# Kernel optimization log

Hardware: AMD Instinct MI355X
Metric: run time of the kernel (lower is better)

The kernel has to match this reference:

```python
import jax, jax.numpy as jnp
import numpy as np

HID = 768  # hidden_size; feature dim is 2*HID


def setup_inputs() -> dict:
    key = jax.random.key(0)
    k1, k2 = jax.random.split(key)
    B, N, K, total_Q, D = 4, 10, 5, 512, 2 * HID
    support = jax.random.normal(k1, (B, N, K, D), dtype=jnp.float32)
    query = jax.random.normal(k2, (B, total_Q, D), dtype=jnp.float32)
    return {"support": support, "query": query, "N": N, "K": K, "total_Q": total_Q}


def reference(support, query, N, K, total_Q):
    B = support.shape[0]
    D = support.shape[-1]
    # (B, N*K, D)
    S = support.reshape(B, N * K, D)
    # negative squared euclidean distance: broadcast (B,1,NK,D) vs (B,Q,1,D) -> (B,Q,NK)
    dist_sq = -jnp.sum((S[:, None, :, :] - query[:, :, None, :]) ** 2, axis=3)
    dist_sq = dist_sq.reshape(B, total_Q, N, K)
    # query-guided weights: mean over queries, tanh, softmax over K -> (B,N,K,1)
    qgw = jax.nn.softmax(jnp.tanh(jnp.mean(dist_sq, axis=1)), axis=-1)[..., None]
    # weighted aggregation over shots -> (B,N,D)
    agg = jnp.sum(support * qgw, axis=2)
    return agg, qgw
```

## Files before the change

### kernel.cpp

```cpp
#include <hip/hip_runtime.h>
#include <math.h>

constexpr int B = 4;
constexpr int N = 10;
constexpr int K = 5;
constexpr int Q = 512;
constexpr int D = 1536;

constexpr int QBAR_OFF = 0;
constexpr int CSUM_OFF = B * D;

__global__ __launch_bounds__(256) void qstats_kernel(
    const float* __restrict__ query, float* __restrict__ ws) {
    const int tid = threadIdx.x;
    const int d   = blockIdx.y * 256 + tid;
    const int b   = blockIdx.z;
    const int q0  = blockIdx.x * 64;

    const float* qp = query + (size_t)b * Q * D + (size_t)q0 * D + d;
    float acc = 0.f, ssq = 0.f;
#pragma unroll 8
    for (int q = 0; q < 64; ++q) {
        float v = qp[(size_t)q * D];
        acc += v;
        ssq = fmaf(v, v, ssq);
    }
    atomicAdd(&ws[QBAR_OFF + b * D + d], acc);

    for (int off = 32; off > 0; off >>= 1) ssq += __shfl_down(ssq, off);
    __shared__ float red[4];
    const int wave = tid >> 6, lane = tid & 63;
    if (lane == 0) red[wave] = ssq;
    __syncthreads();
    if (tid == 0) {
        atomicAdd(&ws[CSUM_OFF + b], red[0] + red[1] + red[2] + red[3]);
    }
}

__global__ __launch_bounds__(256) void agg_kernel(
    const float* __restrict__ support, const float* __restrict__ ws,
    float* __restrict__ out) {
    const int tid = threadIdx.x;
    const int bn  = blockIdx.x;
    const int b   = bn / N;

    const float* sup  = support + (size_t)bn * K * D;
    const float* qbar = ws + QBAR_OFF + (size_t)b * D;

    __shared__ float s_red[2][K][4];
    __shared__ float s_w[K];

    const int wave = tid >> 6, lane = tid & 63;

    for (int k = 0; k < K; ++k) {
        float a = 0.f, c = 0.f;
        for (int d = tid; d < D; d += 256) {
            float s = sup[k * D + d];
            a = fmaf(s, s, a);
            c = fmaf(s, qbar[d], c);
        }
        for (int off = 32; off > 0; off >>= 1) {
            a += __shfl_down(a, off);
            c += __shfl_down(c, off);
        }
        if (lane == 0) { s_red[0][k][wave] = a; s_red[1][k][wave] = c; }
    }
    __syncthreads();

    if (tid < K) {
        const int k = tid;
        float ssk = s_red[0][k][0] + s_red[0][k][1] + s_red[0][k][2] + s_red[0][k][3];
        float sqk = s_red[1][k][0] + s_red[1][k][1] + s_red[1][k][2] + s_red[1][k][3];
        float cb  = ws[CSUM_OFF + b] * (1.f / Q);
        float m = -ssk + 2.f * sqk * (1.f / Q) - cb;
        s_w[k] = tanhf(m);
    }
    __syncthreads();
    if (tid == 0) {
        float mx = s_w[0];
        for (int k = 1; k < K; ++k) mx = fmaxf(mx, s_w[k]);
        float e[K], sum = 0.f;
        for (int k = 0; k < K; ++k) { e[k] = expf(s_w[k] - mx); sum += e[k]; }
        float inv = 1.f / sum;
        for (int k = 0; k < K; ++k) s_w[k] = e[k] * inv;
    }
    __syncthreads();

    if (tid < K) out[(size_t)B * N * D + bn * K + tid] = s_w[tid];

    float w[K];
#pragma unroll
    for (int k = 0; k < K; ++k) w[k] = s_w[k];

    for (int d = tid; d < D; d += 256) {
        float acc = 0.f;
#pragma unroll
        for (int k = 0; k < K; ++k) acc = fmaf(sup[k * D + d], w[k], acc);
        out[(size_t)bn * D + d] = acc;
    }
}

extern "C" void kernel_launch(void* const* d_in, const int* in_sizes, int n_in,
                              void* d_out, int out_size, void* d_ws, size_t ws_size,
                              hipStream_t stream) {
    const float* support = (const float*)d_in[0];
    const float* query   = (const float*)d_in[1];
    float* out = (float*)d_out;
    float* ws  = (float*)d_ws;

    hipMemsetAsync(d_ws, 0, (size_t)(B * D + B) * sizeof(float), stream);

    dim3 g1(Q / 64, D / 256, B);
    qstats_kernel<<<g1, 256, 0, stream>>>(query, ws);

    agg_kernel<<<B * N, 256, 0, stream>>>(support, ws, out);
}
```

Before: 86.90 us.

## Replace atomics and memset with per-chunk partial sums and float4 query loads

Result: slower. 88.92 us (+2.3%).

```diff
diff --git a/kernel.cpp b/kernel.cpp
--- a/kernel.cpp
+++ b/kernel.cpp
@@ -7,34 +7,38 @@
 constexpr int Q = 512;
 constexpr int D = 1536;
 
-constexpr int QBAR_OFF = 0;
-constexpr int CSUM_OFF = B * D;
+constexpr int QCH = 8;
+constexpr int DCH = 3;
+constexpr int CS_OFF = B * QCH * D;
 
-__global__ __launch_bounds__(256) void qstats_kernel(
+__global__ __launch_bounds__(128) void qstats_kernel(
     const float* __restrict__ query, float* __restrict__ ws) {
     const int tid = threadIdx.x;
-    const int d   = blockIdx.y * 256 + tid;
+    const int qch = blockIdx.x;
+    const int dch = blockIdx.y;
     const int b   = blockIdx.z;
-    const int q0  = blockIdx.x * 64;
+    const int c   = dch * 128 + tid;
+    const int d   = c * 4;
 
-    const float* qp = query + (size_t)b * Q * D + (size_t)q0 * D + d;
-    float acc = 0.f, ssq = 0.f;
-#pragma unroll 8
+    const float4* qp =
+        (const float4*)(query + (size_t)b * Q * D + (size_t)qch * 64 * D + d);
+    float4 acc = {0.f, 0.f, 0.f, 0.f};
+    float ssq = 0.f;
+#pragma unroll 4
     for (int q = 0; q < 64; ++q) {
-        float v = qp[(size_t)q * D];
-        acc += v;
-        ssq = fmaf(v, v, ssq);
+        float4 v = qp[q * (D / 4)];
+        acc.x += v.x; acc.y += v.y; acc.z += v.z; acc.w += v.w;
+        ssq = fmaf(v.x, v.x, fmaf(v.y, v.y, fmaf(v.z, v.z, fmaf(v.w, v.w, ssq))));
     }
-    atomicAdd(&ws[QBAR_OFF + b * D + d], acc);
+    float4* pp = (float4*)(ws + (size_t)(b * QCH + qch) * D + d);
+    *pp = acc;
 
     for (int off = 32; off > 0; off >>= 1) ssq += __shfl_down(ssq, off);
-    __shared__ float red[4];
+    __shared__ float red[2];
     const int wave = tid >> 6, lane = tid & 63;
     if (lane == 0) red[wave] = ssq;
     __syncthreads();
-    if (tid == 0) {
-        atomicAdd(&ws[CSUM_OFF + b], red[0] + red[1] + red[2] + red[3]);
-    }
+    if (tid == 0) ws[CS_OFF + (b * QCH + qch) * DCH + dch] = red[0] + red[1];
 }
 
 __global__ __launch_bounds__(256) void agg_kernel(
@@ -44,20 +48,33 @@
     const int bn  = blockIdx.x;
     const int b   = bn / N;
 
-    const float* sup  = support + (size_t)bn * K * D;
-    const float* qbar = ws + QBAR_OFF + (size_t)b * D;
+    const float* sup = support + (size_t)bn * K * D;
 
+    __shared__ float s_qbar[D];
     __shared__ float s_red[2][K][4];
-    __shared__ float s_w[K];
+    __shared__ float s_w[K + 1];
+
+    for (int d = tid; d < D; d += 256) {
+        float s = 0.f;
+#pragma unroll
+        for (int j = 0; j < QCH; ++j) s += ws[(size_t)(b * QCH + j) * D + d];
+        s_qbar[d] = s;
+    }
+    if (tid == 0) {
+        float c = 0.f;
+#pragma unroll
+        for (int j = 0; j < QCH * DCH; ++j) c += ws[CS_OFF + b * QCH * DCH + j];
+        s_w[K] = c;
+    }
+    __syncthreads();
 
     const int wave = tid >> 6, lane = tid & 63;
-
     for (int k = 0; k < K; ++k) {
         float a = 0.f, c = 0.f;
         for (int d = tid; d < D; d += 256) {
             float s = sup[k * D + d];
             a = fmaf(s, s, a);
-            c = fmaf(s, qbar[d], c);
+            c = fmaf(s, s_qbar[d], c);
         }
         for (int off = 32; off > 0; off >>= 1) {
             a += __shfl_down(a, off);
@@ -71,7 +88,7 @@
         const int k = tid;
         float ssk = s_red[0][k][0] + s_red[0][k][1] + s_red[0][k][2] + s_red[0][k][3];
         float sqk = s_red[1][k][0] + s_red[1][k][1] + s_red[1][k][2] + s_red[1][k][3];
-        float cb  = ws[CSUM_OFF + b] * (1.f / Q);
+        float cb  = s_w[K] * (1.f / Q);
         float m = -ssk + 2.f * sqk * (1.f / Q) - cb;
         s_w[k] = tanhf(m);
     }
@@ -108,10 +125,8 @@
     float* out = (float*)d_out;
     float* ws  = (float*)d_ws;
 
-    hipMemsetAsync(d_ws, 0, (size_t)(B * D + B) * sizeof(float), stream);
-
-    dim3 g1(Q / 64, D / 256, B);
-    qstats_kernel<<<g1, 256, 0, stream>>>(query, ws);
+    dim3 g1(QCH, DCH, B);
+    qstats_kernel<<<g1, 128, 0, stream>>>(query, ws);
 
     agg_kernel<<<B * N, 256, 0, stream>>>(support, ws, out);
 }
```
